# Performance work log

Hardware: AMD Instinct MI355X
Metric: run time of the kernel (lower is better)

## Reference

```python
import jax, jax.numpy as jnp
import numpy as np

B, D_IN, D_H = 128, 1024, 1024


def setup_inputs() -> dict:
    key = jax.random.key(0)
    ks = jax.random.split(key, 12)
    scale = 0.02  # small init so exp() input gate stays numerically tame

    def w(k, shape):
        return jax.random.normal(k, shape, dtype=jnp.float32) * scale

    return {
        # forward inputs / carried state
        "x_t": jax.random.normal(ks[0], (B, D_IN), dtype=jnp.float32),
        "C_prev": jax.random.normal(ks[1], (B, D_H, D_H), dtype=jnp.float32) * 0.1,
        "n_prev": jax.random.uniform(ks[2], (B, D_H), dtype=jnp.float32),
        # q/k/v/o projections [input_size, hidden_size] + biases
        "W_q": w(ks[3], (D_IN, D_H)), "b_q": jnp.zeros((D_H,), jnp.float32),
        "W_k": w(ks[4], (D_IN, D_H)), "b_k": jnp.zeros((D_H,), jnp.float32),
        "W_v": w(ks[5], (D_IN, D_H)), "b_v": jnp.zeros((D_H,), jnp.float32),
        "W_o": w(ks[6], (D_IN, D_H)), "b_o": jnp.zeros((D_H,), jnp.float32),
        # scalar i/f gates per example: [input_size] -> scalar
        "w_i": w(ks[7], (D_IN,)), "b_i": jnp.zeros((), jnp.float32),
        "w_f": w(ks[8], (D_IN,)), "b_f": jnp.zeros((), jnp.float32),
    }


def reference(x_t, C_prev, n_prev, W_q, b_q, W_k, b_k, W_v, b_v, W_o, b_o,
              w_i, b_i, w_f, b_f):
    d = W_k.shape[1]
    inv_sqrt_d = 1.0 / jnp.sqrt(jnp.asarray(d, x_t.dtype))

    q = x_t @ W_q + b_q                       # [B, d]
    k = (x_t @ W_k + b_k) * inv_sqrt_d        # [B, d]
    v = x_t @ W_v + b_v                       # [B, d]

    i_t = jnp.exp(x_t @ w_i + b_i)[:, None]           # [B, 1] exponential input gate
    f_t = jax.nn.sigmoid(x_t @ w_f + b_f)[:, None]    # [B, 1] forget gate
    o_t = jax.nn.sigmoid(x_t @ W_o + b_o)             # [B, d] output gate

    # matrix cell-state update: C_t = f*C_{t-1} + i * v k^T
    C_t = f_t[..., None] * C_prev + i_t[..., None] * (v[:, :, None] * k[:, None, :])
    # normalizer state: n_t = f*n_{t-1} + i*k
    n_t = f_t * n_prev + i_t * k

    # h_t = o * (C_t q / max(|n_t^T q|, 1))
    num = jnp.einsum("bde,be->bd", C_t, q)
    den = jnp.maximum(jnp.abs(jnp.einsum("bd,bd->b", n_t, q)), 1.0)[:, None]
    h_t = o_t * (num / den)
    return h_t, C_t, n_t
```

## Files before the change

### kernel.cpp

```cpp
#include <hip/hip_runtime.h>
#include <hip/hip_bf16.h>

#define BATCH 128
#define DIM   1024
#define BD    (BATCH*DIM)
#define CSZ   ((size_t)BD*DIM)

typedef float vf4 __attribute__((ext_vector_type(4)));

__device__ __forceinline__ float sigmoidf_(float z){ return 1.0f/(1.0f+expf(-z)); }
__device__ __forceinline__ float dot4(float4 a, float4 b){
  return a.x*b.x + a.y*b.y + a.z*b.z + a.w*b.w;
}

__global__ void gates_k(const float* __restrict__ x,  const float* __restrict__ wi,
                        const float* __restrict__ bi, const float* __restrict__ wf,
                        const float* __restrict__ bf, float* __restrict__ gI,
                        float* __restrict__ gF){
  __shared__ float red[8];
  const int b = blockIdx.x, tid = threadIdx.x;
  const float4 xv  = *(const float4*)(x  + b*DIM + tid*4);
  const float4 wi4 = *(const float4*)(wi + tid*4);
  const float4 wf4 = *(const float4*)(wf + tid*4);
  float si = dot4(xv, wi4);
  float sf = dot4(xv, wf4);
  #pragma unroll
  for(int off=32; off; off>>=1){ si += __shfl_xor(si,off); sf += __shfl_xor(sf,off); }
  const int w = tid >> 6;
  if((tid & 63) == 0){ red[w] = si; red[4+w] = sf; }
  __syncthreads();
  if(tid == 0){
    float a = red[0]+red[1]+red[2]+red[3];
    float c = red[4]+red[5]+red[6]+red[7];
    gI[b] = expf(a + bi[0]);
    gF[b] = sigmoidf_(c + bf[0]);
  }
}

__global__ __launch_bounds__(256) void gemm_k(
    const float* __restrict__ x,
    const float* __restrict__ w0, const float* __restrict__ w1,
    const float* __restrict__ w2, const float* __restrict__ w3,
    float* __restrict__ part, int KS){
  __shared__ float xs[128][17];
  __shared__ float wsh[16][64];
  const int bx  = blockIdx.x;
  const int ks  = bx >> 6;
  const int ct  = bx & 63;
  const int m   = ct >> 4;
  const int cb  = ct & 15;
  const float* W = (m==0) ? w0 : (m==1) ? w1 : (m==2) ? w2 : w3;
  const int Ksub = DIM / KS;
  const int kb   = ks * Ksub;
  const int tid  = threadIdx.x;
  const int cc = tid & 15, rr = tid >> 4;

  float acc[8][4];
  #pragma unroll
  for(int i=0;i<8;i++)
    #pragma unroll
    for(int j=0;j<4;j++) acc[i][j] = 0.0f;

  for(int kk = 0; kk < Ksub; kk += 16){
    #pragma unroll
    for(int jj=0;jj<2;jj++){
      const int l = tid + jj*256;
      const int row = l >> 2, kc = (l & 3) * 4;
      const float4 v = *(const float4*)(x + row*DIM + kb + kk + kc);
      xs[row][kc+0]=v.x; xs[row][kc+1]=v.y; xs[row][kc+2]=v.z; xs[row][kc+3]=v.w;
    }
    {
      const int kr = tid >> 4, c = (tid & 15) * 4;
      *(float4*)&wsh[kr][c] =
          *(const float4*)(W + (size_t)(kb + kk + kr)*DIM + cb*64 + c);
    }
    __syncthreads();
    #pragma unroll
    for(int t=0;t<16;t++){
      const float4 wa = *(const float4*)&wsh[t][cc*4];
      float xr[8];
      #pragma unroll
      for(int i=0;i<8;i++) xr[i] = xs[rr*8+i][t];
      #pragma unroll
      for(int i=0;i<8;i++){
        acc[i][0] += xr[i]*wa.x; acc[i][1] += xr[i]*wa.y;
        acc[i][2] += xr[i]*wa.z; acc[i][3] += xr[i]*wa.w;
      }
    }
    __syncthreads();
  }

  float* po = part + (size_t)(ks*4 + m) * BD;
  #pragma unroll
  for(int i=0;i<8;i++){
    const int row = rr*8 + i;
    *(float4*)(po + row*DIM + cb*64 + cc*4) =
        make_float4(acc[i][0],acc[i][1],acc[i][2],acc[i][3]);
  }
}

__global__ void combine_k(const float* __restrict__ part,
                          const float* __restrict__ bq, const float* __restrict__ bk,
                          const float* __restrict__ bv, const float* __restrict__ bo,
                          float* __restrict__ qkvo, int KS){
  const int gid  = blockIdx.x*blockDim.x + threadIdx.x;
  const int flat = gid * 4;
  const int m    = flat >> 17;
  const int idx  = flat & (BD - 1);
  const int c    = idx & (DIM - 1);
  float4 s = make_float4(0.f,0.f,0.f,0.f);
  for(int ks=0; ks<KS; ks++){
    const float4 p = *(const float4*)(part + (size_t)(ks*4+m)*BD + idx);
    s.x += p.x; s.y += p.y; s.z += p.z; s.w += p.w;
  }
  const float* bp = (m==0) ? bq : (m==1) ? bk : (m==2) ? bv : bo;
  const float4 bb = *(const float4*)(bp + c);
  s.x += bb.x; s.y += bb.y; s.z += bb.z; s.w += bb.w;
  if(m == 1){
    s.x *= 0.03125f; s.y *= 0.03125f; s.z *= 0.03125f; s.w *= 0.03125f;
  } else if(m == 3){
    s.x = sigmoidf_(s.x); s.y = sigmoidf_(s.y);
    s.z = sigmoidf_(s.z); s.w = sigmoidf_(s.w);
  }
  *(float4*)(qkvo + (size_t)m*BD + idx) = s;
}

__global__ void nden_k(const float* __restrict__ qkvo, const float* __restrict__ nprev,
                       const float* __restrict__ gI, const float* __restrict__ gF,
                       float* __restrict__ nout, float* __restrict__ gD){
  __shared__ float red[4];
  const int b = blockIdx.x, tid = threadIdx.x;
  const float it = gI[b], ft = gF[b];
  const float4 q4 = *(const float4*)(qkvo +            b*DIM + tid*4);
  const float4 k4 = *(const float4*)(qkvo + BD +       b*DIM + tid*4);
  const float4 np = *(const float4*)(nprev +           b*DIM + tid*4);
  float4 n4;
  n4.x = ft*np.x + it*k4.x; n4.y = ft*np.y + it*k4.y;
  n4.z = ft*np.z + it*k4.z; n4.w = ft*np.w + it*k4.w;
  *(float4*)(nout + b*DIM + tid*4) = n4;
  float s = dot4(n4, q4);
  #pragma unroll
  for(int off=32; off; off>>=1) s += __shfl_xor(s, off);
  if((tid & 63) == 0) red[tid>>6] = s;
  __syncthreads();
  if(tid == 0) gD[b] = fmaxf(fabsf(red[0]+red[1]+red[2]+red[3]), 1.0f);
}

__global__ __launch_bounds__(256) void cell_k(
    const float* __restrict__ Cp, float* __restrict__ Co,
    const float* __restrict__ qkvo,
    const float* __restrict__ gI, const float* __restrict__ gF,
    const float* __restrict__ gD, float* __restrict__ hout){
  __shared__ float qs[DIM];
  __shared__ float ksh[DIM];
  const int tid = threadIdx.x;
  const int r0  = blockIdx.x * 16;
  const int b   = r0 >> 10;
  const float* qb = qkvo +        b*DIM;
  const float* kb = qkvo + BD +   b*DIM;
  *(vf4*)&qs [tid*4] = *(const vf4*)(qb + tid*4);
  *(vf4*)&ksh[tid*4] = *(const vf4*)(kb + tid*4);

  const int lane = tid & 63;
  const int wr0  = r0 + ((tid >> 6) << 2);
  const int d0   = wr0 & (DIM - 1);
  const float ft = gF[b], it = gI[b];
  const float rden = 1.0f / gD[b];
  const float* vb = qkvo + 2*BD + b*DIM;
  const float* ob = qkvo + 3*BD + b*DIM;
  const float iv0 = it*vb[d0], iv1 = it*vb[d0+1], iv2 = it*vb[d0+2], iv3 = it*vb[d0+3];
  __syncthreads();

  float a0=0.f, a1=0.f, a2=0.f, a3=0.f;
  const size_t base = (size_t)wr0 * DIM;
  #pragma unroll
  for(int t=0;t<4;t++){
    const int e = (t<<8) + (lane<<2);
    const vf4 q4 = *(const vf4*)&qs [e];
    const vf4 k4 = *(const vf4*)&ksh[e];
    const vf4 c0 = __builtin_nontemporal_load((const vf4*)(Cp + base +         e));
    const vf4 c1 = __builtin_nontemporal_load((const vf4*)(Cp + base + DIM +   e));
    const vf4 c2 = __builtin_nontemporal_load((const vf4*)(Cp + base + 2*DIM + e));
    const vf4 c3 = __builtin_nontemporal_load((const vf4*)(Cp + base + 3*DIM + e));
    const vf4 t0 = ft*c0 + iv0*k4;
    const vf4 t1 = ft*c1 + iv1*k4;
    const vf4 t2 = ft*c2 + iv2*k4;
    const vf4 t3 = ft*c3 + iv3*k4;
    __builtin_nontemporal_store(t0, (vf4*)(Co + base +         e));
    __builtin_nontemporal_store(t1, (vf4*)(Co + base + DIM +   e));
    __builtin_nontemporal_store(t2, (vf4*)(Co + base + 2*DIM + e));
    __builtin_nontemporal_store(t3, (vf4*)(Co + base + 3*DIM + e));
    a0 += t0.x*q4.x + t0.y*q4.y + t0.z*q4.z + t0.w*q4.w;
    a1 += t1.x*q4.x + t1.y*q4.y + t1.z*q4.z + t1.w*q4.w;
    a2 += t2.x*q4.x + t2.y*q4.y + t2.z*q4.z + t2.w*q4.w;
    a3 += t3.x*q4.x + t3.y*q4.y + t3.z*q4.z + t3.w*q4.w;
  }
  #pragma unroll
  for(int off=32; off; off>>=1){
    a0 += __shfl_xor(a0, off); a1 += __shfl_xor(a1, off);
    a2 += __shfl_xor(a2, off); a3 += __shfl_xor(a3, off);
  }
  if(lane == 0){
    float4 h;
    h.x = ob[d0+0]*a0*rden; h.y = ob[d0+1]*a1*rden;
    h.z = ob[d0+2]*a2*rden; h.w = ob[d0+3]*a3*rden;
    *(float4*)(hout + wr0) = h;
  }
}

extern "C" void kernel_launch(void* const* d_in, const int* in_sizes, int n_in,
                              void* d_out, int out_size, void* d_ws, size_t ws_size,
                              hipStream_t stream){
  const float* x  = (const float*)d_in[0];
  const float* Cp = (const float*)d_in[1];
  const float* np = (const float*)d_in[2];
  const float* Wq = (const float*)d_in[3];  const float* bq = (const float*)d_in[4];
  const float* Wk = (const float*)d_in[5];  const float* bk = (const float*)d_in[6];
  const float* Wv = (const float*)d_in[7];  const float* bv = (const float*)d_in[8];
  const float* Wo = (const float*)d_in[9];  const float* bo = (const float*)d_in[10];
  const float* wi = (const float*)d_in[11]; const float* bi = (const float*)d_in[12];
  const float* wf = (const float*)d_in[13]; const float* bf = (const float*)d_in[14];

  float* out  = (float*)d_out;
  float* hout = out;
  float* Cout = out + BD;
  float* nout = out + BD + CSZ;

  int KS = 8;
  size_t need8 = ((size_t)8*4*BD + 4*BD + 384) * 4;
  size_t need2 = ((size_t)2*4*BD + 4*BD + 384) * 4;
  if(ws_size >= need8)      KS = 8;
  else if(ws_size >= need2) KS = 2;
  else                      KS = 1;

  float* part = (float*)d_ws;
  float* qkvo = part + (size_t)KS*4*BD;
  float* gI   = qkvo + (size_t)4*BD;
  float* gF   = gI + BATCH;
  float* gD   = gF + BATCH;

  gates_k  <<<BATCH, 256, 0, stream>>>(x, wi, bi, wf, bf, gI, gF);
  gemm_k   <<<64*KS, 256, 0, stream>>>(x, Wq, Wk, Wv, Wo, part, KS);
  combine_k<<<512,   256, 0, stream>>>(part, bq, bk, bv, bo, qkvo, KS);
  nden_k   <<<BATCH, 256, 0, stream>>>(qkvo, np, gI, gF, nout, gD);
  cell_k   <<<8192,  256, 0, stream>>>(Cp, Cout, qkvo, gI, gF, gD, hout);
}
```

Before: 235.6 us.

## Fuse gate kernel into normalizer kernel, transpose GEMM x tile, coarsen cell blocks

```diff
diff --git a/kernel.cpp b/kernel.cpp
--- a/kernel.cpp
+++ b/kernel.cpp
@@ -5,36 +5,13 @@
 #define DIM   1024
 #define BD    (BATCH*DIM)
 #define CSZ   ((size_t)BD*DIM)
+#define CROWS 64
 
 typedef float vf4 __attribute__((ext_vector_type(4)));
 
 __device__ __forceinline__ float sigmoidf_(float z){ return 1.0f/(1.0f+expf(-z)); }
 __device__ __forceinline__ float dot4(float4 a, float4 b){
   return a.x*b.x + a.y*b.y + a.z*b.z + a.w*b.w;
-}
-
-__global__ void gates_k(const float* __restrict__ x,  const float* __restrict__ wi,
-                        const float* __restrict__ bi, const float* __restrict__ wf,
-                        const float* __restrict__ bf, float* __restrict__ gI,
-                        float* __restrict__ gF){
-  __shared__ float red[8];
-  const int b = blockIdx.x, tid = threadIdx.x;
-  const float4 xv  = *(const float4*)(x  + b*DIM + tid*4);
-  const float4 wi4 = *(const float4*)(wi + tid*4);
-  const float4 wf4 = *(const float4*)(wf + tid*4);
-  float si = dot4(xv, wi4);
-  float sf = dot4(xv, wf4);
-  #pragma unroll
-  for(int off=32; off; off>>=1){ si += __shfl_xor(si,off); sf += __shfl_xor(sf,off); }
-  const int w = tid >> 6;
-  if((tid & 63) == 0){ red[w] = si; red[4+w] = sf; }
-  __syncthreads();
-  if(tid == 0){
-    float a = red[0]+red[1]+red[2]+red[3];
-    float c = red[4]+red[5]+red[6]+red[7];
-    gI[b] = expf(a + bi[0]);
-    gF[b] = sigmoidf_(c + bf[0]);
-  }
 }
 
 __global__ __launch_bounds__(256) void gemm_k(
@@ -42,7 +19,7 @@
     const float* __restrict__ w0, const float* __restrict__ w1,
     const float* __restrict__ w2, const float* __restrict__ w3,
     float* __restrict__ part, int KS){
-  __shared__ float xs[128][17];
+  __shared__ float xst[16][132];
   __shared__ float wsh[16][64];
   const int bx  = blockIdx.x;
   const int ks  = bx >> 6;
@@ -67,7 +44,7 @@
       const int l = tid + jj*256;
       const int row = l >> 2, kc = (l & 3) * 4;
       const float4 v = *(const float4*)(x + row*DIM + kb + kk + kc);
-      xs[row][kc+0]=v.x; xs[row][kc+1]=v.y; xs[row][kc+2]=v.z; xs[row][kc+3]=v.w;
+      xst[kc+0][row]=v.x; xst[kc+1][row]=v.y; xst[kc+2][row]=v.z; xst[kc+3][row]=v.w;
     }
     {
       const int kr = tid >> 4, c = (tid & 15) * 4;
@@ -78,9 +55,11 @@
     #pragma unroll
     for(int t=0;t<16;t++){
       const float4 wa = *(const float4*)&wsh[t][cc*4];
+      const float4 xa = *(const float4*)&xst[t][rr*8];
+      const float4 xb = *(const float4*)&xst[t][rr*8+4];
       float xr[8];
-      #pragma unroll
-      for(int i=0;i<8;i++) xr[i] = xs[rr*8+i][t];
+      xr[0]=xa.x; xr[1]=xa.y; xr[2]=xa.z; xr[3]=xa.w;
+      xr[4]=xb.x; xr[5]=xb.y; xr[6]=xb.z; xr[7]=xb.w;
       #pragma unroll
       for(int i=0;i<8;i++){
         acc[i][0] += xr[i]*wa.x; acc[i][1] += xr[i]*wa.y;
@@ -125,15 +104,36 @@
   *(float4*)(qkvo + (size_t)m*BD + idx) = s;
 }
 
-__global__ void nden_k(const float* __restrict__ qkvo, const float* __restrict__ nprev,
-                       const float* __restrict__ gI, const float* __restrict__ gF,
+__global__ void gfnd_k(const float* __restrict__ x,  const float* __restrict__ wi,
+                       const float* __restrict__ bi, const float* __restrict__ wf,
+                       const float* __restrict__ bf, const float* __restrict__ qkvo,
+                       const float* __restrict__ nprev,
+                       float* __restrict__ gI, float* __restrict__ gF,
                        float* __restrict__ nout, float* __restrict__ gD){
-  __shared__ float red[4];
+  __shared__ float red[8];
+  __shared__ float sif[2];
   const int b = blockIdx.x, tid = threadIdx.x;
-  const float it = gI[b], ft = gF[b];
-  const float4 q4 = *(const float4*)(qkvo +            b*DIM + tid*4);
-  const float4 k4 = *(const float4*)(qkvo + BD +       b*DIM + tid*4);
-  const float4 np = *(const float4*)(nprev +           b*DIM + tid*4);
+  const float4 xv  = *(const float4*)(x  + b*DIM + tid*4);
+  const float4 wi4 = *(const float4*)(wi + tid*4);
+  const float4 wf4 = *(const float4*)(wf + tid*4);
+  float si = dot4(xv, wi4);
+  float sf = dot4(xv, wf4);
+  #pragma unroll
+  for(int off=32; off; off>>=1){ si += __shfl_xor(si,off); sf += __shfl_xor(sf,off); }
+  if((tid & 63) == 0){ red[tid>>6] = si; red[4+(tid>>6)] = sf; }
+  __syncthreads();
+  if(tid == 0){
+    float a = red[0]+red[1]+red[2]+red[3];
+    float c = red[4]+red[5]+red[6]+red[7];
+    float itv = expf(a + bi[0]);
+    float ftv = sigmoidf_(c + bf[0]);
+    gI[b] = itv; gF[b] = ftv; sif[0] = itv; sif[1] = ftv;
+  }
+  __syncthreads();
+  const float it = sif[0], ft = sif[1];
+  const float4 q4 = *(const float4*)(qkvo +      b*DIM + tid*4);
+  const float4 k4 = *(const float4*)(qkvo + BD + b*DIM + tid*4);
+  const float4 np = *(const float4*)(nprev +     b*DIM + tid*4);
   float4 n4;
   n4.x = ft*np.x + it*k4.x; n4.y = ft*np.y + it*k4.y;
   n4.z = ft*np.z + it*k4.z; n4.w = ft*np.w + it*k4.w;
@@ -154,57 +154,60 @@
   __shared__ float qs[DIM];
   __shared__ float ksh[DIM];
   const int tid = threadIdx.x;
-  const int r0  = blockIdx.x * 16;
+  const int r0  = blockIdx.x * CROWS;
   const int b   = r0 >> 10;
   const float* qb = qkvo +        b*DIM;
   const float* kb = qkvo + BD +   b*DIM;
   *(vf4*)&qs [tid*4] = *(const vf4*)(qb + tid*4);
   *(vf4*)&ksh[tid*4] = *(const vf4*)(kb + tid*4);
-
-  const int lane = tid & 63;
-  const int wr0  = r0 + ((tid >> 6) << 2);
-  const int d0   = wr0 & (DIM - 1);
   const float ft = gF[b], it = gI[b];
   const float rden = 1.0f / gD[b];
   const float* vb = qkvo + 2*BD + b*DIM;
   const float* ob = qkvo + 3*BD + b*DIM;
-  const float iv0 = it*vb[d0], iv1 = it*vb[d0+1], iv2 = it*vb[d0+2], iv3 = it*vb[d0+3];
-  __syncthreads();
-
-  float a0=0.f, a1=0.f, a2=0.f, a3=0.f;
-  const size_t base = (size_t)wr0 * DIM;
-  #pragma unroll
-  for(int t=0;t<4;t++){
-    const int e = (t<<8) + (lane<<2);
-    const vf4 q4 = *(const vf4*)&qs [e];
-    const vf4 k4 = *(const vf4*)&ksh[e];
-    const vf4 c0 = __builtin_nontemporal_load((const vf4*)(Cp + base +         e));
-    const vf4 c1 = __builtin_nontemporal_load((const vf4*)(Cp + base + DIM +   e));
-    const vf4 c2 = __builtin_nontemporal_load((const vf4*)(Cp + base + 2*DIM + e));
-    const vf4 c3 = __builtin_nontemporal_load((const vf4*)(Cp + base + 3*DIM + e));
-    const vf4 t0 = ft*c0 + iv0*k4;
-    const vf4 t1 = ft*c1 + iv1*k4;
-    const vf4 t2 = ft*c2 + iv2*k4;
-    const vf4 t3 = ft*c3 + iv3*k4;
-    __builtin_nontemporal_store(t0, (vf4*)(Co + base +         e));
-    __builtin_nontemporal_store(t1, (vf4*)(Co + base + DIM +   e));
-    __builtin_nontemporal_store(t2, (vf4*)(Co + base + 2*DIM + e));
-    __builtin_nontemporal_store(t3, (vf4*)(Co + base + 3*DIM + e));
-    a0 += t0.x*q4.x + t0.y*q4.y + t0.z*q4.z + t0.w*q4.w;
-    a1 += t1.x*q4.x + t1.y*q4.y + t1.z*q4.z + t1.w*q4.w;
-    a2 += t2.x*q4.x + t2.y*q4.y + t2.z*q4.z + t2.w*q4.w;
-    a3 += t3.x*q4.x + t3.y*q4.y + t3.z*q4.z + t3.w*q4.w;
-  }
-  #pragma unroll
-  for(int off=32; off; off>>=1){
-    a0 += __shfl_xor(a0, off); a1 += __shfl_xor(a1, off);
-    a2 += __shfl_xor(a2, off); a3 += __shfl_xor(a3, off);
-  }
-  if(lane == 0){
-    float4 h;
-    h.x = ob[d0+0]*a0*rden; h.y = ob[d0+1]*a1*rden;
-    h.z = ob[d0+2]*a2*rden; h.w = ob[d0+3]*a3*rden;
-    *(float4*)(hout + wr0) = h;
+  const int lane = tid & 63;
+  const int w    = tid >> 6;
+  __syncthreads();
+
+  for(int g = 0; g < 4; ++g){
+    const int wr0 = r0 + g*16 + (w << 2);
+    const int d0  = wr0 & (DIM - 1);
+    const float iv0 = it*vb[d0],   iv1 = it*vb[d0+1];
+    const float iv2 = it*vb[d0+2], iv3 = it*vb[d0+3];
+    float a0=0.f, a1=0.f, a2=0.f, a3=0.f;
+    const size_t base = (size_t)wr0 * DIM;
+    #pragma unroll
+    for(int t=0;t<4;t++){
+      const int e = (t<<8) + (lane<<2);
+      const vf4 q4 = *(const vf4*)&qs [e];
+      const vf4 k4 = *(const vf4*)&ksh[e];
+      const vf4 c0 = *(const vf4*)(Cp + base +         e);
+      const vf4 c1 = *(const vf4*)(Cp + base + DIM +   e);
+      const vf4 c2 = *(const vf4*)(Cp + base + 2*DIM + e);
+      const vf4 c3 = *(const vf4*)(Cp + base + 3*DIM + e);
+      const vf4 t0 = ft*c0 + iv0*k4;
+      const vf4 t1 = ft*c1 + iv1*k4;
+      const vf4 t2 = ft*c2 + iv2*k4;
+      const vf4 t3 = ft*c3 + iv3*k4;
+      __builtin_nontemporal_store(t0, (vf4*)(Co + base +         e));
+      __builtin_nontemporal_store(t1, (vf4*)(Co + base + DIM +   e));
+      __builtin_nontemporal_store(t2, (vf4*)(Co + base + 2*DIM + e));
+      __builtin_nontemporal_store(t3, (vf4*)(Co + base + 3*DIM + e));
+      a0 += t0.x*q4.x + t0.y*q4.y + t0.z*q4.z + t0.w*q4.w;
+      a1 += t1.x*q4.x + t1.y*q4.y + t1.z*q4.z + t1.w*q4.w;
+      a2 += t2.x*q4.x + t2.y*q4.y + t2.z*q4.z + t2.w*q4.w;
+      a3 += t3.x*q4.x + t3.y*q4.y + t3.z*q4.z + t3.w*q4.w;
+    }
+    #pragma unroll
+    for(int off=32; off; off>>=1){
+      a0 += __shfl_xor(a0, off); a1 += __shfl_xor(a1, off);
+      a2 += __shfl_xor(a2, off); a3 += __shfl_xor(a3, off);
+    }
+    if(lane == 0){
+      float4 h;
+      h.x = ob[d0+0]*a0*rden; h.y = ob[d0+1]*a1*rden;
+      h.z = ob[d0+2]*a2*rden; h.w = ob[d0+3]*a3*rden;
+      *(float4*)(hout + wr0) = h;
+    }
   }
 }
 
@@ -239,9 +242,8 @@
   float* gF   = gI + BATCH;
   float* gD   = gF + BATCH;
 
-  gates_k  <<<BATCH, 256, 0, stream>>>(x, wi, bi, wf, bf, gI, gF);
-  gemm_k   <<<64*KS, 256, 0, stream>>>(x, Wq, Wk, Wv, Wo, part, KS);
-  combine_k<<<512,   256, 0, stream>>>(part, bq, bk, bv, bo, qkvo, KS);
-  nden_k   <<<BATCH, 256, 0, stream>>>(qkvo, np, gI, gF, nout, gD);
-  cell_k   <<<8192,  256, 0, stream>>>(Cp, Cout, qkvo, gI, gF, gD, hout);
-}
+  gemm_k   <<<64*KS,   256, 0, stream>>>(x, Wq, Wk, Wv, Wo, part, KS);
+  combine_k<<<512,     256, 0, stream>>>(part, bq, bk, bv, bo, qkvo, KS);
+  gfnd_k   <<<BATCH,   256, 0, stream>>>(x, wi, bi, wf, bf, qkvo, np, gI, gF, nout, gD);
+  cell_k   <<<BD/CROWS,256, 0, stream>>>(Cp, Cout, qkvo, gI, gF, gD, hout);
+}
```

Result: slower. 243.9 us (+3.5%).
